# Kernel optimization log

Hardware: AMD Instinct MI355X
Metric: run time of the kernel (lower is better)

Reference implementation:

```python
import jax, jax.numpy as jnp
import numpy as np

NUM_HEADS = 8

def _feature_map(t):
    return jax.nn.elu(t) + 1.0

def setup_inputs() -> dict:
    key = jax.random.key(0)
    ks = jax.random.split(key, 7)
    B, S, D = 2, 1024, 512
    sc = 1.0 / np.sqrt(D)
    return {
        'x':  jax.random.normal(ks[0], (B, S, D), dtype=jnp.float32),
        'Wq': jax.random.normal(ks[1], (D, D), dtype=jnp.float32) * sc,
        'Wk': jax.random.normal(ks[2], (D, D), dtype=jnp.float32) * sc,
        'Wv': jax.random.normal(ks[3], (D, D), dtype=jnp.float32) * sc,
        'Wo': jax.random.normal(ks[4], (D, D), dtype=jnp.float32) * sc,
        'bo': jnp.zeros((D,), dtype=jnp.float32),
        'Wg': jax.random.normal(ks[5], (2 * D, D), dtype=jnp.float32) * (1.0 / np.sqrt(2 * D)),
        'bg': jnp.zeros((D,), dtype=jnp.float32),
    }

def reference(x, Wq, Wk, Wv, Wo, bo, Wg, bg):
    B, S, D = x.shape
    H = NUM_HEADS
    hd = D // H
    # projections, split heads -> [B,S,H,hd]
    q = _feature_map((x @ Wq).reshape(B, S, H, hd))
    k = _feature_map((x @ Wk).reshape(B, S, H, hd))
    v = (x @ Wv).reshape(B, S, H, hd)
    # causal linear attention via cumulative sums
    kv = jnp.einsum('bshd,bshe->bshde', k, v)        # [B,S,H,hd,hd]
    kv_cumsum = jnp.cumsum(kv, axis=1)
    k_cumsum = jnp.cumsum(k, axis=1)
    numerator = jnp.einsum('bshd,bshde->bshe', q, kv_cumsum)
    denominator = jnp.einsum('bshd,bshd->bsh', q, k_cumsum)[..., None]
    out = (numerator / (denominator + 1e-6)).reshape(B, S, D)
    out = out @ Wo + bo
    gate = jax.nn.sigmoid(jnp.concatenate([x, out], axis=-1) @ Wg + bg)
    return x + gate * (out - x)
```

## Files before the change

kernel.cpp:

```cpp
#include <hip/hip_runtime.h>
#include <hip/hip_bf16.h>
#include <math.h>


typedef __bf16 bf16x8 __attribute__((ext_vector_type(8)));
typedef __bf16 bf16x4 __attribute__((ext_vector_type(4)));
typedef float f32x4 __attribute__((ext_vector_type(4)));

#define MFMA16(a, b, c) __builtin_amdgcn_mfma_f32_16x16x32_bf16(a, b, c, 0, 0, 0)

__device__ __forceinline__ float elu1(float v) { return v > 0.f ? v + 1.f : __expf(v); }

__device__ __forceinline__ void gload16(const void* g, void* l) {
    __builtin_amdgcn_global_load_lds((const __attribute__((address_space(1))) void*)g,
                                     (__attribute__((address_space(3))) void*)l, 16, 0, 0);
}

__global__ __launch_bounds__(256) void prep_kernel(
    const float* __restrict__ x, const float* __restrict__ Wq, const float* __restrict__ Wk,
    const float* __restrict__ Wv, const float* __restrict__ Wo, const float* __restrict__ Wg,
    __bf16* __restrict__ xb, __bf16* __restrict__ wqkvT, __bf16* __restrict__ woT,
    __bf16* __restrict__ wg2T) {
    int z = blockIdx.z;
    if (z == 5) {
        int bid = blockIdx.y * 16 + blockIdx.x;
        int base = (bid * 256 + threadIdx.x) * 8;
        bf16x8 o;
#pragma unroll
        for (int j = 0; j < 8; j++) o[j] = (__bf16)x[base + j];
        *(bf16x8*)&xb[base] = o;
        return;
    }
    const float* in;
    int R = 512;
    if (z == 0) in = Wq;
    else if (z == 1) in = Wk;
    else if (z == 2) in = Wv;
    else if (z == 3) in = Wo;
    else { in = Wg; R = 1024; }
    if ((int)blockIdx.y * 32 >= R) return;
    __shared__ float t[32][33];
    int bx = blockIdx.x, by = blockIdx.y;
    int tx = threadIdx.x & 31, ty = threadIdx.x >> 5;
#pragma unroll
    for (int i = 0; i < 32; i += 8)
        t[ty + i][tx] = in[(size_t)(by * 32 + ty + i) * 512 + bx * 32 + tx];
    __syncthreads();
#pragma unroll
    for (int i = 0; i < 32; i += 8) {
        int n = bx * 32 + ty + i;
        int kk = by * 32 + tx;
        __bf16 val = (__bf16)t[tx][ty + i];
        if (z == 0) wqkvT[(size_t)n * 512 + kk] = val;
        else if (z == 1) wqkvT[(size_t)(512 + n) * 512 + kk] = val;
        else if (z == 2) wqkvT[(size_t)(1024 + n) * 512 + kk] = val;
        else if (z == 3) woT[(size_t)n * 512 + kk] = val;
        else if (kk < 512) wqkvT[(size_t)(1536 + n) * 512 + kk] = val;
        else wg2T[(size_t)n * 512 + (kk - 512)] = val;
    }
}

template <int MODE, int BM, int BN>
__global__ __launch_bounds__(256) void gemm_kernel(
    const __bf16* __restrict__ A, const __bf16* __restrict__ Bw, const float* __restrict__ bias,
    const float* __restrict__ xf, const __bf16* __restrict__ xgb, const __bf16* __restrict__ pvb,
    float* __restrict__ outf, __bf16* __restrict__ outb,
    __bf16* __restrict__ q_out, __bf16* __restrict__ k_out,
    __bf16* __restrict__ kt_out, __bf16* __restrict__ vt_out, __bf16* __restrict__ xg_out, int K) {
    constexpr int MI = BM / 32, NI = BN / 32;
    constexpr int LA = BM / 64, LB = BN / 64;
    constexpr int L = LA + LB;
    __shared__ __bf16 sA[4 * BM * 32];
    __shared__ __bf16 sB[4 * BN * 32];
    __shared__ __bf16 sE[(MODE == 0) ? 64 * 72 : 1];
    int bm = blockIdx.x, bn = blockIdx.y;
    int tid = threadIdx.x, w = tid >> 6, l = tid & 63;
    int wr = (w >> 1) * (16 * MI), wc = (w & 1) * (16 * NI);
    int r = tid >> 2, c = (tid & 3) * 8;
    f32x4 acc[MI][NI] = {};
    const int nt = K / 32;

    auto stage = [&](int t, int buf) {
        int k0 = t * 32;
#pragma unroll
        for (int i = 0; i < LA; i++)
            gload16(&A[(size_t)(bm * BM + i * 64 + r) * K + k0 + c],
                    &sA[buf * (BM * 32) + i * 2048 + w * 512]);
#pragma unroll
        for (int i = 0; i < LB; i++)
            gload16(&Bw[(size_t)(bn * BN + i * 64 + r) * K + k0 + c],
                    &sB[buf * (BN * 32) + i * 2048 + w * 512]);
    };

    stage(0, 0);
    stage(1, 1);
    stage(2, 2);
    for (int t = 0; t < nt; t++) {
        if (t + 2 < nt) {
            if constexpr (L == 2) asm volatile("s_waitcnt vmcnt(4)" ::: "memory");
            else asm volatile("s_waitcnt vmcnt(6)" ::: "memory");
        } else if (t + 1 < nt) {
            if constexpr (L == 2) asm volatile("s_waitcnt vmcnt(2)" ::: "memory");
            else asm volatile("s_waitcnt vmcnt(3)" ::: "memory");
        } else {
            asm volatile("s_waitcnt vmcnt(0)" ::: "memory");
        }
        asm volatile("s_barrier" ::: "memory");
        if (t + 3 < nt) stage(t + 3, (t + 3) & 3);
        int buf = t & 3;
        bf16x8 af[MI], bfr[NI];
#pragma unroll
        for (int mi = 0; mi < MI; mi++)
            af[mi] = *(const bf16x8*)&sA[buf * (BM * 32) + (wr + mi * 16 + (l & 15)) * 32 + ((l >> 4) << 3)];
#pragma unroll
        for (int ni = 0; ni < NI; ni++)
            bfr[ni] = *(const bf16x8*)&sB[buf * (BN * 32) + (wc + ni * 16 + (l & 15)) * 32 + ((l >> 4) << 3)];
#pragma unroll
        for (int mi = 0; mi < MI; mi++)
#pragma unroll
            for (int ni = 0; ni < NI; ni++)
                acc[mi][ni] = MFMA16(af[mi], bfr[ni], acc[mi][ni]);
    }

    if (MODE == 0) {
        __syncthreads();
#pragma unroll
        for (int mi = 0; mi < MI; mi++)
#pragma unroll
            for (int ni = 0; ni < NI; ni++)
#pragma unroll
                for (int j = 0; j < 4; j++) {
                    int lr = wr + mi * 16 + ((l >> 4) << 2) + j;
                    int lc = wc + ni * 16 + (l & 15);
                    float v = acc[mi][ni][j];
                    if (bn < 16) v = elu1(v);
                    sE[lr * 72 + lc] = (__bf16)v;
                }
        __syncthreads();
        int which = bn >> 3;
        int b = bm >> 4, s0b = (bm & 15) * 64, h = bn & 7;
        int bh = b * 8 + h;
        if (which == 0 || which == 1) {
            __bf16* qk = (which == 0 ? q_out : k_out) + ((size_t)(bh * 1024 + s0b)) * 64;
#pragma unroll
            for (int p = 0; p < 2; p++) {
                int idx = p * 256 + tid;
                *(bf16x8*)&qk[idx * 8] = *(const bf16x8*)&sE[(idx >> 3) * 72 + (idx & 7) * 8];
            }
        }
        if (which == 1 || which == 2) {
            __bf16* tdst = (which == 1 ? kt_out : vt_out) + (size_t)(bh * 64) * 1024 + s0b;
            alignas(16) __bf16 tmp[16];
#pragma unroll
            for (int sj = 0; sj < 16; sj++) tmp[sj] = sE[(w * 16 + sj) * 72 + l];
            *(bf16x8*)&tdst[(size_t)l * 1024 + w * 16] = *(const bf16x8*)&tmp[0];
            *(bf16x8*)&tdst[(size_t)l * 1024 + w * 16 + 8] = *(const bf16x8*)&tmp[8];
        }
        if (which == 3) {
            __bf16* dst = xg_out + (size_t)(bm * 64) * 512 + (bn - 24) * 64;
#pragma unroll
            for (int p = 0; p < 2; p++) {
                int idx = p * 256 + tid;
                *(bf16x8*)&dst[(size_t)(idx >> 3) * 512 + (idx & 7) * 8] =
                    *(const bf16x8*)&sE[(idx >> 3) * 72 + (idx & 7) * 8];
            }
        }
    } else {
#pragma unroll
        for (int mi = 0; mi < MI; mi++)
#pragma unroll
            for (int ni = 0; ni < NI; ni++)
#pragma unroll
                for (int j = 0; j < 4; j++) {
                    int gm = bm * BM + wr + mi * 16 + ((l >> 4) << 2) + j;
                    int gn = bn * BN + wc + ni * 16 + (l & 15);
                    if (MODE == 1) {
                        float v = acc[mi][ni][j] + bias[gn];
                        outb[(size_t)gm * 512 + gn] = (__bf16)v;
                    } else {
                        float v = acc[mi][ni][j] + (float)xgb[(size_t)gm * 512 + gn] + bias[gn];
                        float g = 1.f / (1.f + __expf(-v));
                        float xv = xf[(size_t)gm * 512 + gn];
                        float pv = (float)pvb[(size_t)gm * 512 + gn];
                        outf[(size_t)gm * 512 + gn] = xv + g * (pv - xv);
                    }
                }
    }
}

__global__ __launch_bounds__(256) void mc_kernel(const __bf16* __restrict__ ktb,
                                                 const __bf16* __restrict__ vtb,
                                                 float* __restrict__ Mc, float* __restrict__ ksc) {
    int blk = blockIdx.x;
    int bh = blk >> 3, ch = blk & 7;
    int tid = threadIdx.x, w = tid >> 6, l = tid & 63;
    const __bf16* vb = vtb + (size_t)bh * 65536 + ch * 128;
    const __bf16* kp = ktb + (size_t)bh * 65536 + ch * 128;
    f32x4 macc[4] = {};
#pragma unroll
    for (int ks = 0; ks < 4; ks++) {
        bf16x8 a = *(const bf16x8*)&vb[(size_t)(w * 16 + (l & 15)) * 1024 + ks * 32 + ((l >> 4) << 3)];
#pragma unroll
        for (int ni = 0; ni < 4; ni++) {
            bf16x8 bb = *(const bf16x8*)&kp[(size_t)(ni * 16 + (l & 15)) * 1024 + ks * 32 + ((l >> 4) << 3)];
            macc[ni] = MFMA16(a, bb, macc[ni]);
        }
    }
    float* mout = Mc + (size_t)blk * 4096;
#pragma unroll
    for (int ni = 0; ni < 4; ni++)
#pragma unroll
        for (int j = 0; j < 4; j++)
            mout[(size_t)(w * 16 + ((l >> 4) << 2) + j) * 64 + ni * 16 + (l & 15)] = macc[ni][j];
    if (tid < 64) {
        float s = 0.f;
        const __bf16* kr = ktb + (size_t)(bh * 64 + tid) * 1024 + ch * 128;
#pragma unroll
        for (int t = 0; t < 16; t++) {
            bf16x8 v = *(const bf16x8*)&kr[t * 8];
#pragma unroll
            for (int j = 0; j < 8; j++) s += (float)v[j];
        }
        ksc[blk * 64 + tid] = s;
    }
}

__global__ __launch_bounds__(256) void attn_kernel(
    const __bf16* __restrict__ qb, const __bf16* __restrict__ kb,
    const __bf16* __restrict__ vtb, const float* __restrict__ Mc,
    const float* __restrict__ ksc, __bf16* __restrict__ attn_out) {
    int blk = blockIdx.x;
    int bh = blk >> 4, ch = (blk >> 1) & 7, half = blk & 1;
    int b = bh >> 3, h = bh & 7;
    int tid = threadIdx.x, w = tid >> 6, l = tid & 63;

    __shared__ __bf16 sQ[64 * 72];
    __shared__ __bf16 sP[64 * 136];
    __shared__ __bf16 sM[64 * 72];
    __shared__ float den[64];
    __shared__ float rsum[64];
    __shared__ float ksst[64];

    const __bf16* qsrc = qb + (size_t)(bh * 1024 + ch * 128 + half * 64) * 64;
#pragma unroll
    for (int i = 0; i < 2; i++) {
        int e = i * 2048 + tid * 8;
        *(bf16x8*)&sQ[(e >> 6) * 72 + (e & 63)] = *(const bf16x8*)&qsrc[e];
    }
    {
        int r0 = tid >> 2, c0 = (tid & 3) * 16;
        f32x4 s0 = {}, s1 = {}, s2 = {}, s3 = {};
        const float* mcb = Mc + (size_t)(bh * 8) * 4096 + r0 * 64 + c0;
        for (int c = 0; c < ch; c++) {
            const float* p = mcb + (size_t)c * 4096;
            s0 += *(const f32x4*)&p[0];
            s1 += *(const f32x4*)&p[4];
            s2 += *(const f32x4*)&p[8];
            s3 += *(const f32x4*)&p[12];
        }
        __bf16* d = &sM[r0 * 72 + c0];
#pragma unroll
        for (int j = 0; j < 4; j++) {
            d[j] = (__bf16)s0[j];
            d[4 + j] = (__bf16)s1[j];
            d[8 + j] = (__bf16)s2[j];
            d[12 + j] = (__bf16)s3[j];
        }
    }
    if (tid < 64) {
        float s = 0.f;
        for (int c = 0; c < ch; c++) s += ksc[(bh * 8 + c) * 64 + tid];
        ksst[tid] = s;
    }
    __syncthreads();

    if (tid < 64) {
        float s = 0.f;
#pragma unroll
        for (int d0 = 0; d0 < 64; d0 += 8) {
            bf16x8 qv = *(const bf16x8*)&sQ[tid * 72 + d0];
#pragma unroll
            for (int jj = 0; jj < 8; jj++) s += (float)qv[jj] * ksst[d0 + jj];
        }
        den[tid] = s;
    }

    {
        int wr = w * 16;
        const int CFMAX = half ? (w + 4) : w;
        const int CFLIM = half ? 7 : 3;
        const __bf16* kbase = kb + (size_t)(bh * 1024 + ch * 128) * 64;
        bf16x8 aq[2];
#pragma unroll
        for (int ks = 0; ks < 2; ks++)
            aq[ks] = *(const bf16x8*)&sQ[(wr + (l & 15)) * 72 + ks * 32 + ((l >> 4) << 3)];
        f32x4 acc[8] = {};
#pragma unroll
        for (int cf = 0; cf < 8; cf++) {
            if (cf <= CFMAX && cf <= CFLIM) {
#pragma unroll
                for (int ks = 0; ks < 2; ks++) {
                    bf16x8 bfr = *(const bf16x8*)&kbase[(size_t)(cf * 16 + (l & 15)) * 64 + ks * 32 + ((l >> 4) << 3)];
                    acc[cf] = MFMA16(aq[ks], bfr, acc[cf]);
                }
            }
        }
#pragma unroll
        for (int j = 0; j < 4; j++) {
            int lrow = wr + ((l >> 4) << 2) + j;
            int grow = half * 64 + lrow;
            float rs = 0.f;
#pragma unroll
            for (int cf = 0; cf < 8; cf++) {
                if (cf <= CFMAX && cf <= CFLIM) {
                    int col = cf * 16 + (l & 15);
                    float v = acc[cf][j];
                    v = (col <= grow) ? v : 0.f;
                    rs += v;
                    sP[lrow * 136 + col] = (__bf16)v;
                }
            }
            if (CFMAX + 1 <= CFLIM) sP[lrow * 136 + (CFMAX + 1) * 16 + (l & 15)] = (__bf16)0.f;
#pragma unroll
            for (int off = 1; off < 16; off <<= 1) rs += __shfl_xor(rs, off);
            if ((l & 15) == 0) rsum[lrow] = rs;
        }
    }
    __syncthreads();

    f32x4 o[4] = {};
    {
        int wr = w * 16;
        int ksmax = half ? (2 + (w >> 1)) : (w >> 1);
        const __bf16* vbase = vtb + (size_t)bh * 65536 + ch * 128;
#pragma unroll
        for (int ks = 0; ks < 4; ks++) {
            if (ks <= ksmax) {
                bf16x8 a = *(const bf16x8*)&sP[(wr + (l & 15)) * 136 + ks * 32 + ((l >> 4) << 3)];
#pragma unroll
                for (int ni = 0; ni < 4; ni++) {
                    bf16x8 bfr = *(const bf16x8*)&vbase[(size_t)(ni * 16 + (l & 15)) * 1024 + ks * 32 + ((l >> 4) << 3)];
                    o[ni] = MFMA16(a, bfr, o[ni]);
                }
            }
        }
        if (ch > 0) {
#pragma unroll
            for (int ks = 0; ks < 2; ks++) {
                bf16x8 a = *(const bf16x8*)&sQ[(wr + (l & 15)) * 72 + ks * 32 + ((l >> 4) << 3)];
#pragma unroll
                for (int ni = 0; ni < 4; ni++) {
                    bf16x8 bfr = *(const bf16x8*)&sM[(ni * 16 + (l & 15)) * 72 + ks * 32 + ((l >> 4) << 3)];
                    o[ni] = MFMA16(a, bfr, o[ni]);
                }
            }
        }
    }

    __bf16* obase = attn_out + ((size_t)(b * 1024 + ch * 128 + half * 64)) * 512 + h * 64;
#pragma unroll
    for (int j = 0; j < 4; j++) {
        int lrow = w * 16 + ((l >> 4) << 2) + j;
        float dn = den[lrow] + rsum[lrow] + 1e-6f;
#pragma unroll
        for (int ni = 0; ni < 4; ni++) {
            int col = ni * 16 + (l & 15);
            obase[(size_t)lrow * 512 + col] = (__bf16)(o[ni][j] / dn);
        }
    }
}

extern "C" void kernel_launch(void* const* d_in, const int* in_sizes, int n_in,
                              void* d_out, int out_size, void* d_ws, size_t ws_size,
                              hipStream_t stream) {
    const float* x = (const float*)d_in[0];
    const float* Wq = (const float*)d_in[1];
    const float* Wk = (const float*)d_in[2];
    const float* Wv = (const float*)d_in[3];
    const float* Wo = (const float*)d_in[4];
    const float* bo = (const float*)d_in[5];
    const float* Wg = (const float*)d_in[6];
    const float* bg = (const float*)d_in[7];
    float* out = (float*)d_out;

    char* ws = (char*)d_ws;
    size_t off = 0;
    auto alloc = [&](size_t bytes) -> void* {
        void* p = ws + off;
        off += (bytes + 255) & ~(size_t)255;
        return p;
    };
    __bf16* xb    = (__bf16*)alloc((size_t)2048 * 512 * 2);
    __bf16* wqkvT = (__bf16*)alloc((size_t)2048 * 512 * 2);
    __bf16* woT   = (__bf16*)alloc((size_t)512 * 512 * 2);
    __bf16* wg2T  = (__bf16*)alloc((size_t)512 * 512 * 2);
    __bf16* qb    = (__bf16*)alloc((size_t)16 * 1024 * 64 * 2);
    __bf16* kb    = (__bf16*)alloc((size_t)16 * 1024 * 64 * 2);
    __bf16* ktb   = (__bf16*)alloc((size_t)16 * 64 * 1024 * 2);
    __bf16* vtb   = (__bf16*)alloc((size_t)16 * 64 * 1024 * 2);
    float*  Mc    = (float*)alloc((size_t)128 * 4096 * 4);
    float*  ksc   = (float*)alloc((size_t)128 * 64 * 4);
    __bf16* attn  = (__bf16*)alloc((size_t)2048 * 512 * 2);
    __bf16* projb = (__bf16*)alloc((size_t)2048 * 512 * 2);
    __bf16* xgb   = (__bf16*)alloc((size_t)2048 * 512 * 2);

    prep_kernel<<<dim3(16, 32, 6), 256, 0, stream>>>(x, Wq, Wk, Wv, Wo, Wg, xb, wqkvT, woT, wg2T);
    gemm_kernel<0, 64, 64><<<dim3(32, 32), 256, 0, stream>>>(
        xb, wqkvT, nullptr, nullptr, nullptr, nullptr, nullptr, nullptr,
        qb, kb, ktb, vtb, xgb, 512);
    mc_kernel<<<128, 256, 0, stream>>>(ktb, vtb, Mc, ksc);
    attn_kernel<<<256, 256, 0, stream>>>(qb, kb, vtb, Mc, ksc, attn);
    gemm_kernel<1, 64, 64><<<dim3(32, 8), 256, 0, stream>>>(
        attn, woT, bo, nullptr, nullptr, nullptr, nullptr, projb,
        nullptr, nullptr, nullptr, nullptr, nullptr, 512);
    gemm_kernel<2, 64, 64><<<dim3(32, 8), 256, 0, stream>>>(
        projb, wg2T, bg, x, xgb, projb, out, nullptr,
        nullptr, nullptr, nullptr, nullptr, nullptr, 512);
}
```

Before: 62.98 us.

## Merge mc+attn and proj+gate kernels using global flag-based inter-block sync

Result: slower. 121.1 us (+92.2%).

```diff
diff --git a/kernel.cpp b/kernel.cpp
--- a/kernel.cpp
+++ b/kernel.cpp
@@ -8,6 +8,7 @@
 typedef float f32x4 __attribute__((ext_vector_type(4)));
 
 #define MFMA16(a, b, c) __builtin_amdgcn_mfma_f32_16x16x32_bf16(a, b, c, 0, 0, 0)
+#define FLAG_MAGIC 0x13572468u
 
 __device__ __forceinline__ float elu1(float v) { return v > 0.f ? v + 1.f : __expf(v); }
 
@@ -60,178 +61,103 @@
     }
 }
 
-template <int MODE, int BM, int BN>
-__global__ __launch_bounds__(256) void gemm_kernel(
-    const __bf16* __restrict__ A, const __bf16* __restrict__ Bw, const float* __restrict__ bias,
-    const float* __restrict__ xf, const __bf16* __restrict__ xgb, const __bf16* __restrict__ pvb,
-    float* __restrict__ outf, __bf16* __restrict__ outb,
+__global__ __launch_bounds__(256) void qkv_kernel(
+    const __bf16* __restrict__ A, const __bf16* __restrict__ Bw,
     __bf16* __restrict__ q_out, __bf16* __restrict__ k_out,
-    __bf16* __restrict__ kt_out, __bf16* __restrict__ vt_out, __bf16* __restrict__ xg_out, int K) {
-    constexpr int MI = BM / 32, NI = BN / 32;
-    constexpr int LA = BM / 64, LB = BN / 64;
-    constexpr int L = LA + LB;
-    __shared__ __bf16 sA[4 * BM * 32];
-    __shared__ __bf16 sB[4 * BN * 32];
-    __shared__ __bf16 sE[(MODE == 0) ? 64 * 72 : 1];
+    __bf16* __restrict__ kt_out, __bf16* __restrict__ vt_out, __bf16* __restrict__ xg_out,
+    unsigned* __restrict__ flags) {
+    __shared__ __bf16 sA[4 * 64 * 32];
+    __shared__ __bf16 sB[4 * 64 * 32];
+    __shared__ __bf16 sE[64 * 72];
     int bm = blockIdx.x, bn = blockIdx.y;
     int tid = threadIdx.x, w = tid >> 6, l = tid & 63;
-    int wr = (w >> 1) * (16 * MI), wc = (w & 1) * (16 * NI);
+    if (bm == 0 && bn == 0) {
+        for (int i = tid; i < 384; i += 256) flags[i] = 0u;
+    }
+    int wr = (w >> 1) * 32, wc = (w & 1) * 32;
     int r = tid >> 2, c = (tid & 3) * 8;
-    f32x4 acc[MI][NI] = {};
-    const int nt = K / 32;
+    f32x4 acc[2][2] = {};
+    const int nt = 16;
 
     auto stage = [&](int t, int buf) {
         int k0 = t * 32;
-#pragma unroll
-        for (int i = 0; i < LA; i++)
-            gload16(&A[(size_t)(bm * BM + i * 64 + r) * K + k0 + c],
-                    &sA[buf * (BM * 32) + i * 2048 + w * 512]);
-#pragma unroll
-        for (int i = 0; i < LB; i++)
-            gload16(&Bw[(size_t)(bn * BN + i * 64 + r) * K + k0 + c],
-                    &sB[buf * (BN * 32) + i * 2048 + w * 512]);
+        gload16(&A[(size_t)(bm * 64 + r) * 512 + k0 + c], &sA[buf * 2048 + w * 512]);
+        gload16(&Bw[(size_t)(bn * 64 + r) * 512 + k0 + c], &sB[buf * 2048 + w * 512]);
     };
-
     stage(0, 0);
     stage(1, 1);
     stage(2, 2);
     for (int t = 0; t < nt; t++) {
-        if (t + 2 < nt) {
-            if constexpr (L == 2) asm volatile("s_waitcnt vmcnt(4)" ::: "memory");
-            else asm volatile("s_waitcnt vmcnt(6)" ::: "memory");
-        } else if (t + 1 < nt) {
-            if constexpr (L == 2) asm volatile("s_waitcnt vmcnt(2)" ::: "memory");
-            else asm volatile("s_waitcnt vmcnt(3)" ::: "memory");
-        } else {
-            asm volatile("s_waitcnt vmcnt(0)" ::: "memory");
-        }
+        if (t + 2 < nt) asm volatile("s_waitcnt vmcnt(4)" ::: "memory");
+        else if (t + 1 < nt) asm volatile("s_waitcnt vmcnt(2)" ::: "memory");
+        else asm volatile("s_waitcnt vmcnt(0)" ::: "memory");
         asm volatile("s_barrier" ::: "memory");
         if (t + 3 < nt) stage(t + 3, (t + 3) & 3);
         int buf = t & 3;
-        bf16x8 af[MI], bfr[NI];
-#pragma unroll
-        for (int mi = 0; mi < MI; mi++)
-            af[mi] = *(const bf16x8*)&sA[buf * (BM * 32) + (wr + mi * 16 + (l & 15)) * 32 + ((l >> 4) << 3)];
-#pragma unroll
-        for (int ni = 0; ni < NI; ni++)
-            bfr[ni] = *(const bf16x8*)&sB[buf * (BN * 32) + (wc + ni * 16 + (l & 15)) * 32 + ((l >> 4) << 3)];
-#pragma unroll
-        for (int mi = 0; mi < MI; mi++)
-#pragma unroll
-            for (int ni = 0; ni < NI; ni++)
+        bf16x8 af[2], bfr[2];
+#pragma unroll
+        for (int mi = 0; mi < 2; mi++)
+            af[mi] = *(const bf16x8*)&sA[buf * 2048 + (wr + mi * 16 + (l & 15)) * 32 + ((l >> 4) << 3)];
+#pragma unroll
+        for (int ni = 0; ni < 2; ni++)
+            bfr[ni] = *(const bf16x8*)&sB[buf * 2048 + (wc + ni * 16 + (l & 15)) * 32 + ((l >> 4) << 3)];
+#pragma unroll
+        for (int mi = 0; mi < 2; mi++)
+#pragma unroll
+            for (int ni = 0; ni < 2; ni++)
                 acc[mi][ni] = MFMA16(af[mi], bfr[ni], acc[mi][ni]);
     }
 
-    if (MODE == 0) {
-        __syncthreads();
-#pragma unroll
-        for (int mi = 0; mi < MI; mi++)
-#pragma unroll
-            for (int ni = 0; ni < NI; ni++)
-#pragma unroll
-                for (int j = 0; j < 4; j++) {
-                    int lr = wr + mi * 16 + ((l >> 4) << 2) + j;
-                    int lc = wc + ni * 16 + (l & 15);
-                    float v = acc[mi][ni][j];
-                    if (bn < 16) v = elu1(v);
-                    sE[lr * 72 + lc] = (__bf16)v;
-                }
-        __syncthreads();
-        int which = bn >> 3;
-        int b = bm >> 4, s0b = (bm & 15) * 64, h = bn & 7;
-        int bh = b * 8 + h;
-        if (which == 0 || which == 1) {
-            __bf16* qk = (which == 0 ? q_out : k_out) + ((size_t)(bh * 1024 + s0b)) * 64;
-#pragma unroll
-            for (int p = 0; p < 2; p++) {
-                int idx = p * 256 + tid;
-                *(bf16x8*)&qk[idx * 8] = *(const bf16x8*)&sE[(idx >> 3) * 72 + (idx & 7) * 8];
-            }
-        }
-        if (which == 1 || which == 2) {
-            __bf16* tdst = (which == 1 ? kt_out : vt_out) + (size_t)(bh * 64) * 1024 + s0b;
-            alignas(16) __bf16 tmp[16];
-#pragma unroll
-            for (int sj = 0; sj < 16; sj++) tmp[sj] = sE[(w * 16 + sj) * 72 + l];
-            *(bf16x8*)&tdst[(size_t)l * 1024 + w * 16] = *(const bf16x8*)&tmp[0];
-            *(bf16x8*)&tdst[(size_t)l * 1024 + w * 16 + 8] = *(const bf16x8*)&tmp[8];
-        }
-        if (which == 3) {
-            __bf16* dst = xg_out + (size_t)(bm * 64) * 512 + (bn - 24) * 64;
-#pragma unroll
-            for (int p = 0; p < 2; p++) {
-                int idx = p * 256 + tid;
-                *(bf16x8*)&dst[(size_t)(idx >> 3) * 512 + (idx & 7) * 8] =
-                    *(const bf16x8*)&sE[(idx >> 3) * 72 + (idx & 7) * 8];
-            }
-        }
-    } else {
-#pragma unroll
-        for (int mi = 0; mi < MI; mi++)
-#pragma unroll
-            for (int ni = 0; ni < NI; ni++)
-#pragma unroll
-                for (int j = 0; j < 4; j++) {
-                    int gm = bm * BM + wr + mi * 16 + ((l >> 4) << 2) + j;
-                    int gn = bn * BN + wc + ni * 16 + (l & 15);
-                    if (MODE == 1) {
-                        float v = acc[mi][ni][j] + bias[gn];
-                        outb[(size_t)gm * 512 + gn] = (__bf16)v;
-                    } else {
-                        float v = acc[mi][ni][j] + (float)xgb[(size_t)gm * 512 + gn] + bias[gn];
-                        float g = 1.f / (1.f + __expf(-v));
-                        float xv = xf[(size_t)gm * 512 + gn];
-                        float pv = (float)pvb[(size_t)gm * 512 + gn];
-                        outf[(size_t)gm * 512 + gn] = xv + g * (pv - xv);
-                    }
-                }
-    }
-}
-
-__global__ __launch_bounds__(256) void mc_kernel(const __bf16* __restrict__ ktb,
-                                                 const __bf16* __restrict__ vtb,
-                                                 float* __restrict__ Mc, float* __restrict__ ksc) {
+    __syncthreads();
+#pragma unroll
+    for (int mi = 0; mi < 2; mi++)
+#pragma unroll
+        for (int ni = 0; ni < 2; ni++)
+#pragma unroll
+            for (int j = 0; j < 4; j++) {
+                int lr = wr + mi * 16 + ((l >> 4) << 2) + j;
+                int lc = wc + ni * 16 + (l & 15);
+                float v = acc[mi][ni][j];
+                if (bn < 16) v = elu1(v);
+                sE[lr * 72 + lc] = (__bf16)v;
+            }
+    __syncthreads();
+    int which = bn >> 3;
+    int b = bm >> 4, s0b = (bm & 15) * 64, h = bn & 7;
+    int bh = b * 8 + h;
+    if (which == 0 || which == 1) {
+        __bf16* qk = (which == 0 ? q_out : k_out) + ((size_t)(bh * 1024 + s0b)) * 64;
+#pragma unroll
+        for (int p = 0; p < 2; p++) {
+            int idx = p * 256 + tid;
+            *(bf16x8*)&qk[idx * 8] = *(const bf16x8*)&sE[(idx >> 3) * 72 + (idx & 7) * 8];
+        }
+    }
+    if (which == 1 || which == 2) {
+        __bf16* tdst = (which == 1 ? kt_out : vt_out) + (size_t)(bh * 64) * 1024 + s0b;
+        alignas(16) __bf16 tmp[16];
+#pragma unroll
+        for (int sj = 0; sj < 16; sj++) tmp[sj] = sE[(w * 16 + sj) * 72 + l];
+        *(bf16x8*)&tdst[(size_t)l * 1024 + w * 16] = *(const bf16x8*)&tmp[0];
+        *(bf16x8*)&tdst[(size_t)l * 1024 + w * 16 + 8] = *(const bf16x8*)&tmp[8];
+    }
+    if (which == 3) {
+        __bf16* dst = xg_out + (size_t)(bm * 64) * 512 + (bn - 24) * 64;
+#pragma unroll
+        for (int p = 0; p < 2; p++) {
+            int idx = p * 256 + tid;
+            *(bf16x8*)&dst[(size_t)(idx >> 3) * 512 + (idx & 7) * 8] =
+                *(const bf16x8*)&sE[(idx >> 3) * 72 + (idx & 7) * 8];
+        }
+    }
+}
+
+__global__ __launch_bounds__(256) void mcattn_kernel(
+    const __bf16* __restrict__ qb, const __bf16* __restrict__ kb,
+    const __bf16* __restrict__ ktb, const __bf16* __restrict__ vtb,
+    float* __restrict__ Mc, float* __restrict__ ksc, __bf16* __restrict__ attn_out,
+    unsigned* __restrict__ flags) {
     int blk = blockIdx.x;
-    int bh = blk >> 3, ch = blk & 7;
-    int tid = threadIdx.x, w = tid >> 6, l = tid & 63;
-    const __bf16* vb = vtb + (size_t)bh * 65536 + ch * 128;
-    const __bf16* kp = ktb + (size_t)bh * 65536 + ch * 128;
-    f32x4 macc[4] = {};
-#pragma unroll
-    for (int ks = 0; ks < 4; ks++) {
-        bf16x8 a = *(const bf16x8*)&vb[(size_t)(w * 16 + (l & 15)) * 1024 + ks * 32 + ((l >> 4) << 3)];
-#pragma unroll
-        for (int ni = 0; ni < 4; ni++) {
-            bf16x8 bb = *(const bf16x8*)&kp[(size_t)(ni * 16 + (l & 15)) * 1024 + ks * 32 + ((l >> 4) << 3)];
-            macc[ni] = MFMA16(a, bb, macc[ni]);
-        }
-    }
-    float* mout = Mc + (size_t)blk * 4096;
-#pragma unroll
-    for (int ni = 0; ni < 4; ni++)
-#pragma unroll
-        for (int j = 0; j < 4; j++)
-            mout[(size_t)(w * 16 + ((l >> 4) << 2) + j) * 64 + ni * 16 + (l & 15)] = macc[ni][j];
-    if (tid < 64) {
-        float s = 0.f;
-        const __bf16* kr = ktb + (size_t)(bh * 64 + tid) * 1024 + ch * 128;
-#pragma unroll
-        for (int t = 0; t < 16; t++) {
-            bf16x8 v = *(const bf16x8*)&kr[t * 8];
-#pragma unroll
-            for (int j = 0; j < 8; j++) s += (float)v[j];
-        }
-        ksc[blk * 64 + tid] = s;
-    }
-}
-
-__global__ __launch_bounds__(256) void attn_kernel(
-    const __bf16* __restrict__ qb, const __bf16* __restrict__ kb,
-    const __bf16* __restrict__ vtb, const float* __restrict__ Mc,
-    const float* __restrict__ ksc, __bf16* __restrict__ attn_out) {
-    int blk = blockIdx.x;
-    int bh = blk >> 4, ch = (blk >> 1) & 7, half = blk & 1;
-    int b = bh >> 3, h = bh & 7;
     int tid = threadIdx.x, w = tid >> 6, l = tid & 63;
 
     __shared__ __bf16 sQ[64 * 72];
@@ -241,11 +167,59 @@
     __shared__ float rsum[64];
     __shared__ float ksst[64];
 
+    if (blk < 128) {
+        int bh = blk >> 3, ch = blk & 7;
+        const __bf16* vb = vtb + (size_t)bh * 65536 + ch * 128;
+        const __bf16* kp = ktb + (size_t)bh * 65536 + ch * 128;
+        f32x4 macc[4] = {};
+#pragma unroll
+        for (int ks = 0; ks < 4; ks++) {
+            bf16x8 a = *(const bf16x8*)&vb[(size_t)(w * 16 + (l & 15)) * 1024 + ks * 32 + ((l >> 4) << 3)];
+#pragma unroll
+            for (int ni = 0; ni < 4; ni++) {
+                bf16x8 bb = *(const bf16x8*)&kp[(size_t)(ni * 16 + (l & 15)) * 1024 + ks * 32 + ((l >> 4) << 3)];
+                macc[ni] = MFMA16(a, bb, macc[ni]);
+            }
+        }
+        float* mout = Mc + (size_t)blk * 4096;
+#pragma unroll
+        for (int ni = 0; ni < 4; ni++)
+#pragma unroll
+            for (int j = 0; j < 4; j++)
+                mout[(size_t)(w * 16 + ((l >> 4) << 2) + j) * 64 + ni * 16 + (l & 15)] = macc[ni][j];
+        if (tid < 64) {
+            float s = 0.f;
+            const __bf16* kr = ktb + (size_t)(bh * 64 + tid) * 1024 + ch * 128;
+#pragma unroll
+            for (int t = 0; t < 16; t++) {
+                bf16x8 v = *(const bf16x8*)&kr[t * 8];
+#pragma unroll
+                for (int j = 0; j < 8; j++) s += (float)v[j];
+            }
+            ksc[blk * 64 + tid] = s;
+        }
+        __syncthreads();
+        __threadfence();
+        if (tid == 0) atomicExch(&flags[blk], FLAG_MAGIC);
+        return;
+    }
+
+    int ablk = blk - 128;
+    int bh = ablk >> 4, ch = (ablk >> 1) & 7, half = ablk & 1;
+    int b = bh >> 3, h = bh & 7;
+
     const __bf16* qsrc = qb + (size_t)(bh * 1024 + ch * 128 + half * 64) * 64;
 #pragma unroll
     for (int i = 0; i < 2; i++) {
         int e = i * 2048 + tid * 8;
         *(bf16x8*)&sQ[(e >> 6) * 72 + (e & 63)] = *(const bf16x8*)&qsrc[e];
+    }
+    if (ch > 0) {
+        if (tid < ch) {
+            while (atomicAdd(&flags[bh * 8 + tid], 0u) != FLAG_MAGIC) {}
+        }
+        __syncthreads();
+        __threadfence();
     }
     {
         int r0 = tid >> 2, c0 = (tid & 3) * 16;
@@ -367,6 +341,94 @@
             int col = ni * 16 + (l & 15);
             obase[(size_t)lrow * 512 + col] = (__bf16)(o[ni][j] / dn);
         }
+    }
+}
+
+__global__ __launch_bounds__(256) void projgate_kernel(
+    const __bf16* __restrict__ attn, const __bf16* __restrict__ woT,
+    const __bf16* __restrict__ wg2T, const float* __restrict__ bo,
+    const float* __restrict__ bg, const __bf16* __restrict__ xgb,
+    const float* __restrict__ x, __bf16* __restrict__ projb, float* __restrict__ out,
+    unsigned* __restrict__ flags) {
+    __shared__ __bf16 sA[4 * 64 * 32];
+    __shared__ __bf16 sB[4 * 64 * 32];
+    int blk = blockIdx.x;
+    int tid = threadIdx.x, w = tid >> 6, l = tid & 63;
+    int wr = (w >> 1) * 32, wc = (w & 1) * 32;
+    int r = tid >> 2, c = (tid & 3) * 8;
+    const bool is_proj = blk < 256;
+    int pblk = is_proj ? blk : blk - 256;
+    int bm = pblk >> 3, bn = pblk & 7;
+    const __bf16* A = is_proj ? attn : projb;
+    const __bf16* Bw = is_proj ? woT : wg2T;
+
+    if (!is_proj) {
+        if (tid < 8) {
+            while (atomicAdd(&flags[128 + bm * 8 + tid], 0u) != FLAG_MAGIC) {}
+        }
+        __syncthreads();
+        __threadfence();
+    }
+
+    f32x4 acc[2][2] = {};
+    auto stage = [&](int t, int buf) {
+        int k0 = t * 32;
+        gload16(&A[(size_t)(bm * 64 + r) * 512 + k0 + c], &sA[buf * 2048 + w * 512]);
+        gload16(&Bw[(size_t)(bn * 64 + r) * 512 + k0 + c], &sB[buf * 2048 + w * 512]);
+    };
+    stage(0, 0);
+    stage(1, 1);
+    stage(2, 2);
+    for (int t = 0; t < 16; t++) {
+        if (t + 2 < 16) asm volatile("s_waitcnt vmcnt(4)" ::: "memory");
+        else if (t + 1 < 16) asm volatile("s_waitcnt vmcnt(2)" ::: "memory");
+        else asm volatile("s_waitcnt vmcnt(0)" ::: "memory");
+        asm volatile("s_barrier" ::: "memory");
+        if (t + 3 < 16) stage(t + 3, (t + 3) & 3);
+        int buf = t & 3;
+        bf16x8 af[2], bfr[2];
+#pragma unroll
+        for (int mi = 0; mi < 2; mi++)
+            af[mi] = *(const bf16x8*)&sA[buf * 2048 + (wr + mi * 16 + (l & 15)) * 32 + ((l >> 4) << 3)];
+#pragma unroll
+        for (int ni = 0; ni < 2; ni++)
+            bfr[ni] = *(const bf16x8*)&sB[buf * 2048 + (wc + ni * 16 + (l & 15)) * 32 + ((l >> 4) << 3)];
+#pragma unroll
+        for (int mi = 0; mi < 2; mi++)
+#pragma unroll
+            for (int ni = 0; ni < 2; ni++)
+                acc[mi][ni] = MFMA16(af[mi], bfr[ni], acc[mi][ni]);
+    }
+
+    if (is_proj) {
+#pragma unroll
+        for (int mi = 0; mi < 2; mi++)
+#pragma unroll
+            for (int ni = 0; ni < 2; ni++)
+#pragma unroll
+                for (int j = 0; j < 4; j++) {
+                    int gm = bm * 64 + wr + mi * 16 + ((l >> 4) << 2) + j;
+                    int gn = bn * 64 + wc + ni * 16 + (l & 15);
+                    projb[(size_t)gm * 512 + gn] = (__bf16)(acc[mi][ni][j] + bo[gn]);
+                }
+        __syncthreads();
+        __threadfence();
+        if (tid == 0) atomicExch(&flags[128 + pblk], FLAG_MAGIC);
+    } else {
+#pragma unroll
+        for (int mi = 0; mi < 2; mi++)
+#pragma unroll
+            for (int ni = 0; ni < 2; ni++)
+#pragma unroll
+                for (int j = 0; j < 4; j++) {
+                    int gm = bm * 64 + wr + mi * 16 + ((l >> 4) << 2) + j;
+                    int gn = bn * 64 + wc + ni * 16 + (l & 15);
+                    float v = acc[mi][ni][j] + (float)xgb[(size_t)gm * 512 + gn] + bg[gn];
+                    float g = 1.f / (1.f + __expf(-v));
+                    float xv = x[(size_t)gm * 512 + gn];
+                    float pv = (float)projb[(size_t)gm * 512 + gn];
+                    out[(size_t)gm * 512 + gn] = xv + g * (pv - xv);
+                }
     }
 }
 
@@ -403,17 +465,10 @@
     __bf16* attn  = (__bf16*)alloc((size_t)2048 * 512 * 2);
     __bf16* projb = (__bf16*)alloc((size_t)2048 * 512 * 2);
     __bf16* xgb   = (__bf16*)alloc((size_t)2048 * 512 * 2);
+    unsigned* flags = (unsigned*)alloc((size_t)384 * 4);
 
     prep_kernel<<<dim3(16, 32, 6), 256, 0, stream>>>(x, Wq, Wk, Wv, Wo, Wg, xb, wqkvT, woT, wg2T);
-    gemm_kernel<0, 64, 64><<<dim3(32, 32), 256, 0, stream>>>(
-        xb, wqkvT, nullptr, nullptr, nullptr, nullptr, nullptr, nullptr,
-        qb, kb, ktb, vtb, xgb, 512);
-    mc_kernel<<<128, 256, 0, stream>>>(ktb, vtb, Mc, ksc);
-    attn_kernel<<<256, 256, 0, stream>>>(qb, kb, vtb, Mc, ksc, attn);
-    gemm_kernel<1, 64, 64><<<dim3(32, 8), 256, 0, stream>>>(
-        attn, woT, bo, nullptr, nullptr, nullptr, nullptr, projb,
-        nullptr, nullptr, nullptr, nullptr, nullptr, 512);
-    gemm_kernel<2, 64, 64><<<dim3(32, 8), 256, 0, stream>>>(
-        projb, wg2T, bg, x, xgb, projb, out, nullptr,
-        nullptr, nullptr, nullptr, nullptr, nullptr, 512);
-}
+    qkv_kernel<<<dim3(32, 32), 256, 0, stream>>>(xb, wqkvT, qb, kb, ktb, vtb, xgb, flags);
+    mcattn_kernel<<<384, 256, 0, stream>>>(qb, kb, ktb, vtb, Mc, ksc, attn, flags);
+    projgate_kernel<<<512, 256, 0, stream>>>(attn, woT, wg2T, bo, bg, xgb, x, projb, out, flags);
+}
```

## Use BK=64 XOR-swizzled LDS tiles with triple buffering in GEMM kernel

Applied to the files above, without the earlier changes.

After: 58.12 us. 7.7% less time.

```diff
diff --git a/kernel.cpp b/kernel.cpp
--- a/kernel.cpp
+++ b/kernel.cpp
@@ -60,74 +60,75 @@
     }
 }
 
-template <int MODE, int BM, int BN>
+template <int MODE>
 __global__ __launch_bounds__(256) void gemm_kernel(
     const __bf16* __restrict__ A, const __bf16* __restrict__ Bw, const float* __restrict__ bias,
     const float* __restrict__ xf, const __bf16* __restrict__ xgb, const __bf16* __restrict__ pvb,
     float* __restrict__ outf, __bf16* __restrict__ outb,
     __bf16* __restrict__ q_out, __bf16* __restrict__ k_out,
     __bf16* __restrict__ kt_out, __bf16* __restrict__ vt_out, __bf16* __restrict__ xg_out, int K) {
-    constexpr int MI = BM / 32, NI = BN / 32;
-    constexpr int LA = BM / 64, LB = BN / 64;
-    constexpr int L = LA + LB;
-    __shared__ __bf16 sA[4 * BM * 32];
-    __shared__ __bf16 sB[4 * BN * 32];
-    __shared__ __bf16 sE[(MODE == 0) ? 64 * 72 : 1];
+    __shared__ __bf16 sA[3 * 64 * 64];
+    __shared__ __bf16 sB[3 * 64 * 64];
     int bm = blockIdx.x, bn = blockIdx.y;
     int tid = threadIdx.x, w = tid >> 6, l = tid & 63;
-    int wr = (w >> 1) * (16 * MI), wc = (w & 1) * (16 * NI);
-    int r = tid >> 2, c = (tid & 3) * 8;
-    f32x4 acc[MI][NI] = {};
-    const int nt = K / 32;
+    int wr = (w >> 1) * 32, wc = (w & 1) * 32;
+    f32x4 acc[2][2] = {};
+    const int nt = K / 64;
 
     auto stage = [&](int t, int buf) {
-        int k0 = t * 32;
-#pragma unroll
-        for (int i = 0; i < LA; i++)
-            gload16(&A[(size_t)(bm * BM + i * 64 + r) * K + k0 + c],
-                    &sA[buf * (BM * 32) + i * 2048 + w * 512]);
-#pragma unroll
-        for (int i = 0; i < LB; i++)
-            gload16(&Bw[(size_t)(bn * BN + i * 64 + r) * K + k0 + c],
-                    &sB[buf * (BN * 32) + i * 2048 + w * 512]);
+        int k0 = t * 64;
+#pragma unroll
+        for (int i = 0; i < 2; i++) {
+            int row = i * 32 + w * 8 + (l >> 3);
+            int gc = (((l & 7) << 4) ^ ((row & 7) << 4)) >> 1;
+            gload16(&A[(size_t)(bm * 64 + row) * K + k0 + gc],
+                    &sA[buf * 4096 + i * 2048 + w * 512]);
+            gload16(&Bw[(size_t)(bn * 64 + row) * K + k0 + gc],
+                    &sB[buf * 4096 + i * 2048 + w * 512]);
+        }
     };
 
     stage(0, 0);
     stage(1, 1);
-    stage(2, 2);
     for (int t = 0; t < nt; t++) {
-        if (t + 2 < nt) {
-            if constexpr (L == 2) asm volatile("s_waitcnt vmcnt(4)" ::: "memory");
-            else asm volatile("s_waitcnt vmcnt(6)" ::: "memory");
-        } else if (t + 1 < nt) {
-            if constexpr (L == 2) asm volatile("s_waitcnt vmcnt(2)" ::: "memory");
-            else asm volatile("s_waitcnt vmcnt(3)" ::: "memory");
-        } else {
-            asm volatile("s_waitcnt vmcnt(0)" ::: "memory");
-        }
+        if (t + 1 < nt) asm volatile("s_waitcnt vmcnt(4)" ::: "memory");
+        else asm volatile("s_waitcnt vmcnt(0)" ::: "memory");
         asm volatile("s_barrier" ::: "memory");
-        if (t + 3 < nt) stage(t + 3, (t + 3) & 3);
-        int buf = t & 3;
-        bf16x8 af[MI], bfr[NI];
-#pragma unroll
-        for (int mi = 0; mi < MI; mi++)
-            af[mi] = *(const bf16x8*)&sA[buf * (BM * 32) + (wr + mi * 16 + (l & 15)) * 32 + ((l >> 4) << 3)];
-#pragma unroll
-        for (int ni = 0; ni < NI; ni++)
-            bfr[ni] = *(const bf16x8*)&sB[buf * (BN * 32) + (wc + ni * 16 + (l & 15)) * 32 + ((l >> 4) << 3)];
-#pragma unroll
-        for (int mi = 0; mi < MI; mi++)
-#pragma unroll
-            for (int ni = 0; ni < NI; ni++)
-                acc[mi][ni] = MFMA16(af[mi], bfr[ni], acc[mi][ni]);
+        if (t + 2 < nt) stage(t + 2, (t + 2) % 3);
+        int buf = t % 3;
+        bf16x8 af[2][2], bfr[2][2];
+#pragma unroll
+        for (int kk = 0; kk < 2; kk++) {
+            int cb = kk * 64 + ((l >> 4) << 4);
+#pragma unroll
+            for (int mi = 0; mi < 2; mi++) {
+                int rowA = wr + mi * 16 + (l & 15);
+                af[kk][mi] = *(const bf16x8*)&sA[buf * 4096 + rowA * 64 +
+                                                ((cb ^ ((rowA & 7) << 4)) >> 1)];
+            }
+#pragma unroll
+            for (int ni = 0; ni < 2; ni++) {
+                int rowB = wc + ni * 16 + (l & 15);
+                bfr[kk][ni] = *(const bf16x8*)&sB[buf * 4096 + rowB * 64 +
+                                                 ((cb ^ ((rowB & 7) << 4)) >> 1)];
+            }
+        }
+#pragma unroll
+        for (int kk = 0; kk < 2; kk++)
+#pragma unroll
+            for (int mi = 0; mi < 2; mi++)
+#pragma unroll
+                for (int ni = 0; ni < 2; ni++)
+                    acc[mi][ni] = MFMA16(af[kk][mi], bfr[kk][ni], acc[mi][ni]);
     }
 
     if (MODE == 0) {
+        __bf16* sE = sA;
         __syncthreads();
 #pragma unroll
-        for (int mi = 0; mi < MI; mi++)
-#pragma unroll
-            for (int ni = 0; ni < NI; ni++)
+        for (int mi = 0; mi < 2; mi++)
+#pragma unroll
+            for (int ni = 0; ni < 2; ni++)
 #pragma unroll
                 for (int j = 0; j < 4; j++) {
                     int lr = wr + mi * 16 + ((l >> 4) << 2) + j;
@@ -167,13 +168,13 @@
         }
     } else {
 #pragma unroll
-        for (int mi = 0; mi < MI; mi++)
-#pragma unroll
-            for (int ni = 0; ni < NI; ni++)
+        for (int mi = 0; mi < 2; mi++)
+#pragma unroll
+            for (int ni = 0; ni < 2; ni++)
 #pragma unroll
                 for (int j = 0; j < 4; j++) {
-                    int gm = bm * BM + wr + mi * 16 + ((l >> 4) << 2) + j;
-                    int gn = bn * BN + wc + ni * 16 + (l & 15);
+                    int gm = bm * 64 + wr + mi * 16 + ((l >> 4) << 2) + j;
+                    int gn = bn * 64 + wc + ni * 16 + (l & 15);
                     if (MODE == 1) {
                         float v = acc[mi][ni][j] + bias[gn];
                         outb[(size_t)gm * 512 + gn] = (__bf16)v;
@@ -405,15 +406,15 @@
     __bf16* xgb   = (__bf16*)alloc((size_t)2048 * 512 * 2);
 
     prep_kernel<<<dim3(16, 32, 6), 256, 0, stream>>>(x, Wq, Wk, Wv, Wo, Wg, xb, wqkvT, woT, wg2T);
-    gemm_kernel<0, 64, 64><<<dim3(32, 32), 256, 0, stream>>>(
+    gemm_kernel<0><<<dim3(32, 32), 256, 0, stream>>>(
         xb, wqkvT, nullptr, nullptr, nullptr, nullptr, nullptr, nullptr,
         qb, kb, ktb, vtb, xgb, 512);
     mc_kernel<<<128, 256, 0, stream>>>(ktb, vtb, Mc, ksc);
     attn_kernel<<<256, 256, 0, stream>>>(qb, kb, vtb, Mc, ksc, attn);
-    gemm_kernel<1, 64, 64><<<dim3(32, 8), 256, 0, stream>>>(
+    gemm_kernel<1><<<dim3(32, 8), 256, 0, stream>>>(
         attn, woT, bo, nullptr, nullptr, nullptr, nullptr, projb,
         nullptr, nullptr, nullptr, nullptr, nullptr, 512);
-    gemm_kernel<2, 64, 64><<<dim3(32, 8), 256, 0, stream>>>(
+    gemm_kernel<2><<<dim3(32, 8), 256, 0, stream>>>(
         projb, wg2T, bg, x, xgb, projb, out, nullptr,
         nullptr, nullptr, nullptr, nullptr, nullptr, 512);
 }
```
